# Kernel tuning notes

Measured on AMD Instinct MI355X. Metric: run time of the kernel, lower is better.

The kernel has to match this reference:

```python
import jax, jax.numpy as jnp
import numpy as np

HIDDEN = 768
B = 32
GRID_X, GRID_Y = 84, 30          # 84*30 = 2520 input patches
SEQ = GRID_X * GRID_Y            # 2520
OUT_LEN = 280                    # 2520 // 280 = 9 -> k = 3


def setup_inputs() -> dict:
    key = jax.random.key(0)
    k1, k2 = jax.random.split(key)
    hidden_states = jax.random.normal(k1, (B, SEQ, HIDDEN), dtype=jnp.float32)
    # (x, y) grid coordinates for each patch, identical across batch
    x = jnp.arange(SEQ, dtype=jnp.int32) % GRID_X
    y = jnp.arange(SEQ, dtype=jnp.int32) // GRID_X
    pos = jnp.stack([x, y], axis=-1)                     # [SEQ, 2]
    pixel_position_ids = jnp.broadcast_to(pos, (B, SEQ, 2))
    padding_positions = jax.random.bernoulli(k2, 0.05, (B, SEQ))  # bool mask
    return {
        "hidden_states": hidden_states,
        "pixel_position_ids": pixel_position_ids,
        "padding_positions": padding_positions,
        "output_length": OUT_LEN,
    }


def reference(hidden_states, pixel_position_ids, padding_positions, output_length):
    root_hidden_size = hidden_states.shape[-1] ** 0.5
    # zero out padded patches
    hs = jnp.where(padding_positions[..., None], 0.0, hidden_states)
    seq_len = hs.shape[1]
    if seq_len != output_length:
        k = int((seq_len // output_length) ** 0.5)
        k_squared = k * k
        clamped = jnp.maximum(pixel_position_ids, 0)            # [B, S, 2]
        max_x = jnp.max(clamped[..., 0], axis=-1, keepdims=True) + 1  # [B, 1]
        kidx = clamped // k
        seg = kidx[..., 0] + (max_x // k) * kidx[..., 1]        # [B, S] bucket ids
        hs32 = hs.astype(jnp.float32)
        # segment-sum per batch == one_hot(seg).T @ hs, without the dense one-hot
        pooled = jax.vmap(
            lambda h, i: jax.ops.segment_sum(h, i, num_segments=output_length)
        )(hs32, seg) / k_squared                                 # [B, L, H]
        counts = jax.vmap(
            lambda i: jax.ops.segment_sum(jnp.ones_like(i), i, num_segments=output_length)
        )(seg)                                                   # [B, L]
        mask = counts > 0  # bucket received at least one patch (one-hot col nonzero)
        hs = pooled.astype(hidden_states.dtype)
        padding_positions = mask
    hs = hs * root_hidden_size
    return hs, padding_positions
```

## Files before the change

kernel.cpp:

```cpp
#include <hip/hip_runtime.h>
#include <math.h>


#define NB   32
#define SEQL 2520
#define HID  768
#define OUTL 280
#define CAP  16

__global__ void __launch_bounds__(256)
k_prep(const int* __restrict__ pos, const int* __restrict__ padding,
       int* __restrict__ ents, float* __restrict__ out_mask, int k) {
    __shared__ int red[256];
    __shared__ int s_cnt[OUTL];
    __shared__ int s_ent[OUTL * CAP];
    const int b = blockIdx.x;
    const int t = threadIdx.x;
    const int* p = pos + (size_t)b * SEQL * 2;

    int m = 0;
    for (int s = t; s < SEQL; s += 256) {
        int x = p[2 * s];
        if (x < 0) x = 0;
        if (x > m) m = x;
    }
    red[t] = m;
    __syncthreads();
    for (int off = 128; off > 0; off >>= 1) {
        if (t < off) { int o = red[t + off]; if (o > red[t]) red[t] = o; }
        __syncthreads();
    }
    const int mxk = (red[0] + 1) / k;

    for (int i = t; i < OUTL; i += 256) s_cnt[i] = 0;
    for (int i = t; i < OUTL * CAP; i += 256) s_ent[i] = 1;
    __syncthreads();

    const int* pd = padding + (size_t)b * SEQL;
    for (int s = t; s < SEQL; s += 256) {
        int x = p[2 * s];     if (x < 0) x = 0;
        int y = p[2 * s + 1]; if (y < 0) y = 0;
        int seg = x / k + mxk * (y / k);
        if (seg >= 0 && seg < OUTL) {
            int slot = atomicAdd(&s_cnt[seg], 1);
            if (slot < CAP)
                s_ent[seg * CAP + slot] = (s << 1) | (pd[s] != 0 ? 1 : 0);
        }
    }
    __syncthreads();

    int* eg = ents + (size_t)b * OUTL * CAP;
    for (int i = t; i < OUTL * CAP; i += 256) eg[i] = s_ent[i];
    for (int i = t; i < OUTL; i += 256)
        out_mask[b * OUTL + i] = (s_cnt[i] > 0) ? 1.0f : 0.0f;
}

__global__ void __launch_bounds__(192)
k_pool(const float* __restrict__ hs, const int* __restrict__ ents,
       float* __restrict__ out, float scale) {
    __shared__ int se[9];
    const int l = blockIdx.x;
    const int b = blockIdx.y;
    const int bl = b * OUTL + l;

    if (threadIdx.x == 0) {
        int e[9];
        const int* eg = ents + (size_t)bl * CAP;
        #pragma unroll
        for (int i = 0; i < 9; ++i) e[i] = eg[i];
        #pragma unroll
        for (int i = 1; i < 9; ++i) {
            int v = e[i], j = i - 1;
            while (j >= 0 && e[j] > v) { e[j + 1] = e[j]; --j; }
            e[j + 1] = v;
        }
        #pragma unroll
        for (int i = 0; i < 9; ++i) se[i] = e[i];
    }
    __syncthreads();

    float4 acc = make_float4(0.f, 0.f, 0.f, 0.f);
    const float4* base = (const float4*)(hs + (size_t)b * SEQL * HID);
    #pragma unroll
    for (int i = 0; i < 9; ++i) {
        int e = se[i];
        if (!(e & 1)) {
            float4 v = base[(size_t)(e >> 1) * (HID / 4) + threadIdx.x];
            acc.x += v.x; acc.y += v.y; acc.z += v.z; acc.w += v.w;
        }
    }
    acc.x *= scale; acc.y *= scale; acc.z *= scale; acc.w *= scale;
    ((float4*)(out + (size_t)bl * HID))[threadIdx.x] = acc;
}

extern "C" void kernel_launch(void* const* d_in, const int* in_sizes, int n_in,
                              void* d_out, int out_size, void* d_ws, size_t ws_size,
                              hipStream_t stream) {
    const float* hs      = (const float*)d_in[0];
    const int*   pos     = (const int*)d_in[1];
    const int*   padding = (const int*)d_in[2];

    int* ents = (int*)d_ws;

    float* out      = (float*)d_out;
    float* out_mask = out + (size_t)NB * OUTL * HID;
    const float scale = sqrtf((float)HID) / 9.0f;

    k_prep<<<NB, 256, 0, stream>>>(pos, padding, ents, out_mask, 3);
    dim3 grid(OUTL, NB);
    k_pool<<<grid, 192, 0, stream>>>(hs, ents, out, scale);
}
```

Before: 57.52 us.

## Add regular-grid fast path for pooling and use nontemporal loads and stores

Measured after the change: 51.33 us. 1.12x faster.

```diff
diff --git a/kernel.cpp b/kernel.cpp
--- a/kernel.cpp
+++ b/kernel.cpp
@@ -2,45 +2,59 @@
 #include <math.h>
 
 
-#define NB   32
-#define SEQL 2520
-#define HID  768
-#define OUTL 280
-#define CAP  16
+#define NB    32
+#define SEQL  2520
+#define HID   768
+#define OUTL  280
+#define CAP   16
+#define GX    84
+#define KP    3
+#define MXK   (GX / KP)
+
+typedef float f32x4 __attribute__((ext_vector_type(4)));
 
 __global__ void __launch_bounds__(256)
-k_prep(const int* __restrict__ pos, const int* __restrict__ padding,
-       int* __restrict__ ents, float* __restrict__ out_mask, int k) {
-    __shared__ int red[256];
+k_verify(const int* __restrict__ pos, const int* __restrict__ padding,
+         int* __restrict__ flags, int* __restrict__ ents,
+         float* __restrict__ out_mask) {
+    __shared__ int r_ok[256];
+    __shared__ int r_mx[256];
     __shared__ int s_cnt[OUTL];
     __shared__ int s_ent[OUTL * CAP];
     const int b = blockIdx.x;
     const int t = threadIdx.x;
     const int* p = pos + (size_t)b * SEQL * 2;
 
-    int m = 0;
+    int ok = 1, m = 0;
     for (int s = t; s < SEQL; s += 256) {
-        int x = p[2 * s];
-        if (x < 0) x = 0;
-        if (x > m) m = x;
+        int x = p[2 * s], y = p[2 * s + 1];
+        ok &= (x == s % GX) & (y == s / GX);
+        int cx = x < 0 ? 0 : x;
+        if (cx > m) m = cx;
     }
-    red[t] = m;
+    r_ok[t] = ok; r_mx[t] = m;
     __syncthreads();
     for (int off = 128; off > 0; off >>= 1) {
-        if (t < off) { int o = red[t + off]; if (o > red[t]) red[t] = o; }
+        if (t < off) {
+            r_ok[t] &= r_ok[t + off];
+            int o = r_mx[t + off]; if (o > r_mx[t]) r_mx[t] = o;
+        }
         __syncthreads();
     }
-    const int mxk = (red[0] + 1) / k;
+    if (r_ok[0]) {
+        if (t == 0) flags[b] = 1;
+        return;
+    }
 
+    const int mxk = (r_mx[0] + 1) / KP;
     for (int i = t; i < OUTL; i += 256) s_cnt[i] = 0;
     for (int i = t; i < OUTL * CAP; i += 256) s_ent[i] = 1;
     __syncthreads();
-
     const int* pd = padding + (size_t)b * SEQL;
     for (int s = t; s < SEQL; s += 256) {
         int x = p[2 * s];     if (x < 0) x = 0;
         int y = p[2 * s + 1]; if (y < 0) y = 0;
-        int seg = x / k + mxk * (y / k);
+        int seg = x / KP + mxk * (y / KP);
         if (seg >= 0 && seg < OUTL) {
             int slot = atomicAdd(&s_cnt[seg], 1);
             if (slot < CAP)
@@ -48,22 +62,30 @@
         }
     }
     __syncthreads();
-
     int* eg = ents + (size_t)b * OUTL * CAP;
     for (int i = t; i < OUTL * CAP; i += 256) eg[i] = s_ent[i];
     for (int i = t; i < OUTL; i += 256)
         out_mask[b * OUTL + i] = (s_cnt[i] > 0) ? 1.0f : 0.0f;
+    if (t == 0) flags[b] = 0;
 }
 
 __global__ void __launch_bounds__(192)
-k_pool(const float* __restrict__ hs, const int* __restrict__ ents,
-       float* __restrict__ out, float scale) {
+k_pool(const float* __restrict__ hs, const int* __restrict__ padding,
+       const int* __restrict__ flags, const int* __restrict__ ents,
+       float* __restrict__ out, float* __restrict__ out_mask, float scale) {
     __shared__ int se[9];
     const int l = blockIdx.x;
     const int b = blockIdx.y;
     const int bl = b * OUTL + l;
 
-    if (threadIdx.x == 0) {
+    if (flags[b]) {
+        if ((int)threadIdx.x < 9) {
+            int dy = threadIdx.x / 3, dx = threadIdx.x - 3 * dy;
+            int s = (KP * (l / MXK) + dy) * GX + KP * (l % MXK) + dx;
+            se[threadIdx.x] = (s << 1) | (padding[b * SEQL + s] != 0 ? 1 : 0);
+        }
+        if (threadIdx.x == 0) out_mask[bl] = 1.0f;
+    } else if (threadIdx.x == 0) {
         int e[9];
         const int* eg = ents + (size_t)bl * CAP;
         #pragma unroll
@@ -79,18 +101,20 @@
     }
     __syncthreads();
 
-    float4 acc = make_float4(0.f, 0.f, 0.f, 0.f);
-    const float4* base = (const float4*)(hs + (size_t)b * SEQL * HID);
+    f32x4 acc = (f32x4)(0.f);
+    const f32x4* base = (const f32x4*)(hs + (size_t)b * SEQL * HID);
     #pragma unroll
     for (int i = 0; i < 9; ++i) {
         int e = se[i];
         if (!(e & 1)) {
-            float4 v = base[(size_t)(e >> 1) * (HID / 4) + threadIdx.x];
-            acc.x += v.x; acc.y += v.y; acc.z += v.z; acc.w += v.w;
+            f32x4 v = __builtin_nontemporal_load(
+                base + (size_t)(e >> 1) * (HID / 4) + threadIdx.x);
+            acc += v;
         }
     }
-    acc.x *= scale; acc.y *= scale; acc.z *= scale; acc.w *= scale;
-    ((float4*)(out + (size_t)bl * HID))[threadIdx.x] = acc;
+    acc *= scale;
+    __builtin_nontemporal_store(acc,
+        (f32x4*)(out + (size_t)bl * HID) + threadIdx.x);
 }
 
 extern "C" void kernel_launch(void* const* d_in, const int* in_sizes, int n_in,
@@ -100,13 +124,14 @@
     const int*   pos     = (const int*)d_in[1];
     const int*   padding = (const int*)d_in[2];
 
-    int* ents = (int*)d_ws;
+    int* flags = (int*)d_ws;
+    int* ents  = (int*)((char*)d_ws + 128);
 
     float* out      = (float*)d_out;
     float* out_mask = out + (size_t)NB * OUTL * HID;
     const float scale = sqrtf((float)HID) / 9.0f;
 
-    k_prep<<<NB, 256, 0, stream>>>(pos, padding, ents, out_mask, 3);
+    k_verify<<<NB, 256, 0, stream>>>(pos, padding, flags, ents, out_mask);
     dim3 grid(OUTL, NB);
-    k_pool<<<grid, 192, 0, stream>>>(hs, ents, out, scale);
+    k_pool<<<grid, 192, 0, stream>>>(hs, padding, flags, ents, out, out_mask, scale);
 }
```
